# Performance work log

Hardware: AMD Instinct MI355X
Metric: run time of the kernel (lower is better)

The kernel has to match this reference:

```python
import jax, jax.numpy as jnp
import numpy as np

N = 100000   # num_nodes
E = 1600000  # num_edges
DIN = 128
H1 = 256
H2 = 128
SLOPE = 0.01  # torch leaky_relu default negative slope


def _gcn_conv(h, W, b, src, dst):
    # GCNConv: add self-loops, symmetric deg^-1/2 normalization, linear transform, scatter-add, bias
    hw = h @ W  # [N, out]
    loops = jnp.arange(N)
    s = jnp.concatenate([src, loops])
    d = jnp.concatenate([dst, loops])
    deg = jax.ops.segment_sum(jnp.ones(s.shape[0], dtype=hw.dtype), d, num_segments=N)
    dis = jnp.where(deg > 0, jax.lax.rsqrt(deg), 0.0)
    msg = hw[s] * (dis[s] * dis[d])[:, None]
    return jax.ops.segment_sum(msg, d, num_segments=N) + b


def _gru_cell(x, h, Wih, Whh, bih, bhh):
    # torch.nn.GRUCell semantics; weight layout [3H, in], gate order r, z, n
    gi = x @ Wih.T + bih
    gh = h @ Whh.T + bhh
    ir, iz, inn = jnp.split(gi, 3, axis=-1)
    hr, hz, hn = jnp.split(gh, 3, axis=-1)
    r = jax.nn.sigmoid(ir + hr)
    z = jax.nn.sigmoid(iz + hz)
    n = jnp.tanh(inn + r * hn)
    return (1.0 - z) * n + z * h


def setup_inputs() -> dict:
    key = jax.random.key(0)
    ks = jax.random.split(key, 24)
    rn = lambda k, shape, s=0.05: (jax.random.normal(k, shape) * s).astype(jnp.float32)
    return {
        "x": rn(ks[0], (N, DIN), 1.0),
        "edge_index": jax.random.randint(ks[1], (2, E), 0, N, dtype=jnp.int32),
        "prev0": rn(ks[2], (N, H1), 1.0),
        "prev1": rn(ks[3], (N, H2), 1.0),
        "Wp1": rn(ks[4], (DIN, 256)), "bp1": jnp.zeros((256,), jnp.float32),
        "Wp2": rn(ks[5], (256, 128)), "bp2": jnp.zeros((128,), jnp.float32),
        "Wc1": rn(ks[6], (128, H1)), "bc1": jnp.zeros((H1,), jnp.float32),
        "Wc2": rn(ks[7], (H1, H2)), "bc2": jnp.zeros((H2,), jnp.float32),
        "Wih1": rn(ks[8], (3 * H1, H1)), "Whh1": rn(ks[9], (3 * H1, H1)),
        "bih1": jnp.zeros((3 * H1,), jnp.float32), "bhh1": jnp.zeros((3 * H1,), jnp.float32),
        "Wih2": rn(ks[10], (3 * H2, H2)), "Whh2": rn(ks[11], (3 * H2, H2)),
        "bih2": jnp.zeros((3 * H2,), jnp.float32), "bhh2": jnp.zeros((3 * H2,), jnp.float32),
        "Wpost": rn(ks[12], (H2, 2)), "bpost": jnp.zeros((2,), jnp.float32),
    }


def reference(x, edge_index, prev0, prev1, Wp1, bp1, Wp2, bp2, Wc1, bc1, Wc2, bc2,
              Wih1, Whh1, bih1, bhh1, Wih2, Whh2, bih2, bhh2, Wpost, bpost):
    src, dst = edge_index[0], edge_index[1]
    # preprocess MLP (dropout p=0 => identity)
    h = jax.nn.leaky_relu(x @ Wp1 + bp1, SLOPE)
    h = jax.nn.leaky_relu(h @ Wp2 + bp2, SLOPE)
    # GCN layer 1 + GRU temporal update
    h = jax.nn.leaky_relu(_gcn_conv(h, Wc1, bc1, src, dst), SLOPE)
    h = _gru_cell(h, prev0, Wih1, Whh1, bih1, bhh1)
    emb0 = h
    # GCN layer 2 + GRU temporal update
    h = jax.nn.leaky_relu(_gcn_conv(h, Wc2, bc2, src, dst), SLOPE)
    h = _gru_cell(h, prev1, Wih2, Whh2, bih2, bhh2)
    emb1 = h
    # postprocess and reduce
    out = jnp.sum(h @ Wpost + bpost, axis=-1)  # [N]
    return out, emb0, emb1
```

## Files before the change

kernel.cpp:

```cpp
#include <hip/hip_runtime.h>
#include <cstdint>
#include <cstddef>

typedef __bf16 bf16x8 __attribute__((ext_vector_type(8)));
typedef float f32x4 __attribute__((ext_vector_type(4)));
typedef float f32x2 __attribute__((ext_vector_type(2)));
typedef unsigned short us16;

__device__ __forceinline__ float lrelu(float v) { return v >= 0.0f ? v : 0.01f * v; }
__device__ __forceinline__ float fsigmoid(float x) {
  x = fminf(fmaxf(x, -30.0f), 30.0f);
  return 1.0f / (1.0f + __expf(-x));
}
__device__ __forceinline__ float ftanh(float x) {
  x = fminf(fmaxf(x, -15.0f), 15.0f);
  float e = __expf(2.0f * x);
  return (e - 1.0f) / (e + 1.0f);
}
__device__ __forceinline__ us16 f2b(float f) {
  unsigned int u = __builtin_bit_cast(unsigned int, f);
  u = (u + 0x7fffu + ((u >> 16) & 1u)) >> 16;
  return (us16)u;
}
__device__ __forceinline__ float b2f(us16 h) {
  unsigned int u = ((unsigned int)h) << 16;
  return __builtin_bit_cast(float, u);
}
__device__ __forceinline__ unsigned pk2(float a, float b) {
  return (unsigned)f2b(a) | ((unsigned)f2b(b) << 16);
}
__device__ __forceinline__ unsigned char f2f8(float v) {
  return (unsigned char)(__builtin_amdgcn_cvt_pk_fp8_f32(v, v, 0, false) & 0xFF);
}
__device__ __forceinline__ void unpf8(int2 v, float* t) {
  f32x2 p0 = __builtin_amdgcn_cvt_pk_f32_fp8(v.x, false);
  f32x2 p1 = __builtin_amdgcn_cvt_pk_f32_fp8(v.x, true);
  f32x2 p2 = __builtin_amdgcn_cvt_pk_f32_fp8(v.y, false);
  f32x2 p3 = __builtin_amdgcn_cvt_pk_f32_fp8(v.y, true);
  t[0] = p0.x; t[1] = p0.y; t[2] = p1.x; t[3] = p1.y;
  t[4] = p2.x; t[5] = p2.y; t[6] = p3.x; t[7] = p3.y;
}

__device__ __forceinline__ void stage16(const us16* gsrc, us16* ldst) {
  __builtin_amdgcn_global_load_lds(
      (const __attribute__((address_space(1))) unsigned int*)(const void*)gsrc,
      (__attribute__((address_space(3))) unsigned int*)(void*)ldst, 16, 0, 0);
}
__device__ __forceinline__ bf16x8 frag_rd(const us16* base, int row, int byte_in_row) {
  int byte = row * 128 + (byte_in_row ^ ((row & 7) << 4));
  return *(const bf16x8*)((const char*)base + byte);
}
__device__ __forceinline__ bf16x8 frd32(const us16* tilebase, int row, int ck16) {
  int slot = ck16 ^ ((row >> 1) & 3);
  return *(const bf16x8*)(tilebase + row * 32 + slot * 8);
}

__global__ void k_deg(const int* __restrict__ dst, int* __restrict__ indeg, int E) {
  int e = blockIdx.x * 256 + threadIdx.x;
  if (e < E) atomicAdd(&indeg[dst[e]], 1);
}

__global__ __launch_bounds__(1024) void k_scan1(const int* __restrict__ v, int* __restrict__ rp,
                                                int* __restrict__ part, float* __restrict__ dis, int n) {
  __shared__ int wsum[16];
  int base = blockIdx.x << 10;
  int t = threadIdx.x, lane = t & 63, wv = t >> 6;
  int val = (base + t < n) ? v[base + t] : 0;
  if (base + t < n) dis[base + t] = rsqrtf((float)(val + 1));
  int s = val;
  #pragma unroll
  for (int off = 1; off < 64; off <<= 1) {
    int u = __shfl_up(s, off);
    if (lane >= off) s += u;
  }
  if (lane == 63) wsum[wv] = s;
  __syncthreads();
  int wadd = 0;
  #pragma unroll
  for (int w = 0; w < 16; ++w) wadd += (w < wv) ? wsum[w] : 0;
  if (base + t < n) rp[base + t] = wadd + s - val;
  if (t == 0) {
    int tot = 0;
    #pragma unroll
    for (int w = 0; w < 16; ++w) tot += wsum[w];
    part[blockIdx.x] = tot;
  }
}

__global__ __launch_bounds__(1024) void k_scan2(int* __restrict__ p, int nc) {
  __shared__ int wsum[16];
  int t = threadIdx.x, lane = t & 63, wv = t >> 6;
  int val = (t < nc) ? p[t] : 0;
  int s = val;
  #pragma unroll
  for (int off = 1; off < 64; off <<= 1) {
    int u = __shfl_up(s, off);
    if (lane >= off) s += u;
  }
  if (lane == 63) wsum[wv] = s;
  __syncthreads();
  int wadd = 0;
  #pragma unroll
  for (int w = 0; w < 16; ++w) wadd += (w < wv) ? wsum[w] : 0;
  if (t < nc) p[t] = wadd + s - val;
}

__global__ void k_scan3(int* __restrict__ rp, const int* __restrict__ part,
                        int* __restrict__ cursor, int n, int total) {
  int i = blockIdx.x * 256 + threadIdx.x;
  if (i < n) {
    int v = rp[i] + part[i >> 10];
    rp[i] = v;
    cursor[i] = v;
  } else if (i == n) {
    rp[n] = total;
  }
}

__global__ void k_fill(const int* __restrict__ src, const int* __restrict__ dst,
                       const float* __restrict__ dis, int* __restrict__ cursor,
                       int* __restrict__ csrc, float* __restrict__ cw, int E) {
  int e = blockIdx.x * 256 + threadIdx.x;
  if (e >= E) return;
  int s = src[e], d = dst[e];
  int pos = atomicAdd(&cursor[d], 1);
  csrc[pos] = s;
  cw[pos] = dis[s] * dis[d];
}

__global__ void k_cast(const float* __restrict__ in, us16* __restrict__ out, int n) {
  int i = (blockIdx.x * 256 + threadIdx.x) * 4;
  if (i >= n) return;
  float4 v = *(const float4*)(in + i);
  *(ushort4*)(out + i) = make_ushort4(f2b(v.x), f2b(v.y), f2b(v.z), f2b(v.w));
}

__global__ void k_prepw(const float* __restrict__ Wih1, const float* __restrict__ Whh1,
                        const float* __restrict__ Wih2, const float* __restrict__ Whh2,
                        const float* __restrict__ Wp1, const float* __restrict__ Wp2,
                        const float* __restrict__ Wc1, const float* __restrict__ Wc2,
                        us16* __restrict__ Wih1b, us16* __restrict__ Whh1b,
                        us16* __restrict__ Wih2b, us16* __restrict__ Whh2b,
                        us16* __restrict__ WtP1, us16* __restrict__ WtP2,
                        us16* __restrict__ WtC1, us16* __restrict__ WtC2) {
  int e = blockIdx.x * 256 + threadIdx.x;
  if (e < 196608) { Wih1b[e] = f2b(Wih1[e]); return; }
  e -= 196608;
  if (e < 196608) { Whh1b[e] = f2b(Whh1[e]); return; }
  e -= 196608;
  if (e < 49152) { Wih2b[e] = f2b(Wih2[e]); return; }
  e -= 49152;
  if (e < 49152) { Whh2b[e] = f2b(Whh2[e]); return; }
  e -= 49152;
  if (e < 32768) { int r = e & 127, c = e >> 7; WtP1[e] = f2b(Wp1[(size_t)r * 256 + c]); return; }
  e -= 32768;
  if (e < 32768) { int r = e & 255, c = e >> 8; WtP2[e] = f2b(Wp2[(size_t)r * 128 + c]); return; }
  e -= 32768;
  if (e < 32768) { int r = e & 127, c = e >> 7; WtC1[e] = f2b(Wc1[(size_t)r * 256 + c]); return; }
  e -= 32768;
  if (e < 32768) { int r = e & 255, c = e >> 8; WtC2[e] = f2b(Wc2[(size_t)r * 128 + c]); }
}

template<int ACT, int BIAS, int OF8>
__global__ __launch_bounds__(256) void k_mm(const us16* __restrict__ A,
                                            const us16* __restrict__ Bt,
                                            const float* __restrict__ bias,
                                            void* __restrict__ Cout,
                                            int M, int K, int Nc, int ny) {
  __shared__ __align__(16) us16 lds[2][2 * 8192];
  const int bm = (blockIdx.x / ny) * 128;
  const int bn = (blockIdx.x % ny) * 128;
  const int tid = threadIdx.x;
  const int lane = tid & 63;
  const int wave = tid >> 6;
  const int wm = (wave >> 1) * 64;
  const int wn = (wave & 1) * 64;
  const int lr = lane & 15;
  const int lk = lane >> 4;
  const int srow = lane >> 3;
  const int schk = (lane & 7) ^ srow;
  f32x4 acc[4][4] = {};

  auto stage = [&](int k0, us16* buf) {
    #pragma unroll
    for (int it = 0; it < 4; ++it) {
      int r8 = (wave * 4 + it) * 8;
      int ar = bm + r8 + srow; if (ar >= M) ar = M - 1;
      stage16(A + (size_t)ar * K + k0 + schk * 8, buf + r8 * 64);
      stage16(Bt + (size_t)(bn + r8 + srow) * K + k0 + schk * 8, buf + 8192 + r8 * 64);
    }
  };

  const int nk = K >> 6;
  stage(0, lds[0]);
  for (int t = 0; t < nk; ++t) {
    us16* cur = lds[t & 1];
    if (t + 1 < nk) {
      if (t > 0) {
        asm volatile("s_waitcnt lgkmcnt(0)" ::: "memory");
        __builtin_amdgcn_s_barrier();
      }
      stage((t + 1) << 6, lds[(t + 1) & 1]);
      asm volatile("s_waitcnt vmcnt(8)" ::: "memory");
    } else {
      asm volatile("s_waitcnt vmcnt(0)" ::: "memory");
    }
    __builtin_amdgcn_s_barrier();
    #pragma unroll
    for (int kk = 0; kk < 2; ++kk) {
      bf16x8 af[4], bq[4];
      #pragma unroll
      for (int i = 0; i < 4; ++i) af[i] = frag_rd(cur, wm + i * 16 + lr, kk * 64 + lk * 16);
      #pragma unroll
      for (int j = 0; j < 4; ++j) bq[j] = frag_rd(cur + 8192, wn + j * 16 + lr, kk * 64 + lk * 16);
      #pragma unroll
      for (int i = 0; i < 4; ++i)
        #pragma unroll
        for (int j = 0; j < 4; ++j)
          acc[i][j] = __builtin_amdgcn_mfma_f32_16x16x32_bf16(af[i], bq[j], acc[i][j], 0, 0, 0);
    }
  }
  float bb[4];
  #pragma unroll
  for (int j = 0; j < 4; ++j) bb[j] = BIAS ? bias[bn + wn + j * 16 + lr] : 0.0f;
  #pragma unroll
  for (int i = 0; i < 4; ++i) {
    #pragma unroll
    for (int q = 0; q < 4; ++q) {
      int row = bm + wm + i * 16 + lk * 4 + q;
      if (row < M) {
        #pragma unroll
        for (int j = 0; j < 4; ++j) {
          int col = bn + wn + j * 16 + lr;
          float v = acc[i][j][q] + bb[j];
          if (ACT) v = lrelu(v);
          if (OF8) ((unsigned char*)Cout)[(size_t)row * Nc + col] = f2f8(v);
          else ((us16*)Cout)[(size_t)row * Nc + col] = f2b(v);
        }
      }
    }
  }
}

template<int ACT>
__global__ __launch_bounds__(256) void k_agg128(const unsigned char* __restrict__ hw,
                                                const int* __restrict__ rp,
                                                const int* __restrict__ csrc, const float* __restrict__ cw,
                                                const float* __restrict__ dis, const float* __restrict__ bias,
                                                us16* __restrict__ outp, int M) {
  int node = blockIdx.x * 16 + (threadIdx.x >> 4);
  int l = threadIdx.x & 15;
  if (node >= M) return;
  const unsigned char* base = hw + l * 8;
  float acc[8], t0[8], t1[8], t2[8], t3[8];
  float dn = dis[node];
  float sw = dn * dn;
  {
    int2 v = *(const int2*)(base + (size_t)node * 128);
    unpf8(v, t0);
    #pragma unroll
    for (int j = 0; j < 8; ++j) acc[j] = t0[j] * sw;
  }
  int e = rp[node], e1 = rp[node + 1];
  for (; e + 4 <= e1; e += 4) {
    int s0 = csrc[e], s1 = csrc[e + 1], s2 = csrc[e + 2], s3 = csrc[e + 3];
    float w0 = cw[e], w1 = cw[e + 1], w2 = cw[e + 2], w3 = cw[e + 3];
    int2 v0 = *(const int2*)(base + (size_t)s0 * 128);
    int2 v1 = *(const int2*)(base + (size_t)s1 * 128);
    int2 v2 = *(const int2*)(base + (size_t)s2 * 128);
    int2 v3 = *(const int2*)(base + (size_t)s3 * 128);
    unpf8(v0, t0); unpf8(v1, t1); unpf8(v2, t2); unpf8(v3, t3);
    #pragma unroll
    for (int j = 0; j < 8; ++j) acc[j] = fmaf(w0, t0[j], acc[j]);
    #pragma unroll
    for (int j = 0; j < 8; ++j) acc[j] = fmaf(w1, t1[j], acc[j]);
    #pragma unroll
    for (int j = 0; j < 8; ++j) acc[j] = fmaf(w2, t2[j], acc[j]);
    #pragma unroll
    for (int j = 0; j < 8; ++j) acc[j] = fmaf(w3, t3[j], acc[j]);
  }
  for (; e < e1; ++e) {
    int s0 = csrc[e];
    float w0 = cw[e];
    int2 v0 = *(const int2*)(base + (size_t)s0 * 128);
    unpf8(v0, t0);
    #pragma unroll
    for (int j = 0; j < 8; ++j) acc[j] = fmaf(w0, t0[j], acc[j]);
  }
  if (ACT) {
    float4 b0 = *(const float4*)(bias + l * 8);
    float4 b1 = *(const float4*)(bias + l * 8 + 4);
    float bb[8] = {b0.x, b0.y, b0.z, b0.w, b1.x, b1.y, b1.z, b1.w};
    #pragma unroll
    for (int j = 0; j < 8; ++j) acc[j] = lrelu(acc[j] + bb[j]);
  }
  int4 o;
  o.x = (int)pk2(acc[0], acc[1]);
  o.y = (int)pk2(acc[2], acc[3]);
  o.z = (int)pk2(acc[4], acc[5]);
  o.w = (int)pk2(acc[6], acc[7]);
  *(int4*)(outp + (size_t)node * 128 + l * 8) = o;
}

template<int H, int WB, int PH>
__global__ __launch_bounds__(512) void k_fgru(const us16* __restrict__ xb, const us16* __restrict__ hb,
                                              const us16* __restrict__ Wih, const us16* __restrict__ Whh,
                                              const float* __restrict__ bih, const float* __restrict__ bhh,
                                              float* __restrict__ emb, us16* __restrict__ embb,
                                              const float* __restrict__ Wpost, const float* __restrict__ bpost,
                                              float* __restrict__ outv, int M, int ny) {
  __shared__ __align__(16) us16 lds[2][14336];
  const int nwg = gridDim.x;
  int bid = blockIdx.x;
  {
    int q8 = nwg >> 3, r8 = nwg & 7;
    int xc = bid & 7, ix = bid >> 3;
    bid = (xc < r8 ? xc * (q8 + 1) : r8 * (q8 + 1) + (xc - r8) * q8) + ix;
  }
  const int bn = (bid % ny) * 32;
  const int bm = (bid / ny) * 128;
  const int tid = threadIdx.x;
  const int lane = tid & 63, wave = tid >> 6;
  const int pair = wave >> 1;
  const int role = wave & 1;
  const int wm = pair * 32;
  const int lr = lane & 15, lk = lane >> 4;
  const int sl_row = lane >> 2;
  const int sl_chk = (lane & 3) ^ ((lane >> 3) & 3);

  f32x4 acc[3][2][2] = {};

  auto stage_step = [&](int k0, us16* buf) {
    #pragma unroll
    for (int it = 0; it < 4; ++it) {
      int m = wave * 4 + it;
      if (m >= 28) break;
      const us16* src;
      us16* dst;
      if (m < 16) {
        int r0 = (m & 7) * 16;
        int ar = bm + r0 + sl_row; if (ar >= M) ar = M - 1;
        src = (m < 8 ? xb : hb) + (size_t)ar * H + k0 + sl_chk * 8;
        dst = buf + (m < 8 ? 0 : 4096) + r0 * 32;
      } else {
        int wi = m - 16;
        int g6 = wi >> 1;
        int r0 = (wi & 1) * 16;
        const us16* W = (g6 < 3) ? Wih : Whh;
        int gg = (g6 < 3) ? g6 : g6 - 3;
        src = W + (size_t)(gg * H + bn + r0 + sl_row) * H + k0 + sl_chk * 8;
        dst = buf + 8192 + g6 * 1024 + r0 * 32;
      }
      stage16(src, dst);
    }
  };

  const int nk = H >> 5;
  stage_step(0, lds[0]);
  for (int t = 0; t < nk; ++t) {
    us16* cur = lds[t & 1];
    if (t + 1 < nk) {
      if (t > 0) {
        asm volatile("s_waitcnt lgkmcnt(0)" ::: "memory");
        __builtin_amdgcn_s_barrier();
      }
      stage_step((t + 1) << 5, lds[(t + 1) & 1]);
      asm volatile("s_waitcnt vmcnt(4)" ::: "memory");
    } else {
      asm volatile("s_waitcnt vmcnt(0)" ::: "memory");
    }
    __builtin_amdgcn_s_barrier();
    const us16* at = cur + (role ? 4096 : 0);
    bf16x8 a0 = frd32(at, wm + lr, lk);
    bf16x8 a1 = frd32(at, wm + 16 + lr, lk);
    #pragma unroll
    for (int g = 0; g < 3; ++g) {
      const us16* wt = cur + 8192 + (role * 3 + g) * 1024;
      bf16x8 b0 = frd32(wt, lr, lk);
      bf16x8 b1 = frd32(wt, 16 + lr, lk);
      acc[g][0][0] = __builtin_amdgcn_mfma_f32_16x16x32_bf16(a0, b0, acc[g][0][0], 0, 0, 0);
      acc[g][0][1] = __builtin_amdgcn_mfma_f32_16x16x32_bf16(a0, b1, acc[g][0][1], 0, 0, 0);
      acc[g][1][0] = __builtin_amdgcn_mfma_f32_16x16x32_bf16(a1, b0, acc[g][1][0], 0, 0, 0);
      acc[g][1][1] = __builtin_amdgcn_mfma_f32_16x16x32_bf16(a1, b1, acc[g][1][1], 0, 0, 0);
    }
  }
  __syncthreads();
  float* xch = (float*)&lds[0][0];
  if (role) {
    #pragma unroll
    for (int g = 0; g < 3; ++g)
      #pragma unroll
      for (int i = 0; i < 2; ++i)
        #pragma unroll
        for (int j = 0; j < 2; ++j)
          *(f32x4*)&xch[((((pair * 3 + g) * 2 + i) * 2 + j) * 64 + lane) * 4] = acc[g][i][j];
  }
  __syncthreads();
  if (!role) {
    float part[2][4] = {};
    #pragma unroll
    for (int j = 0; j < 2; ++j) {
      int col = bn + j * 16 + lr;
      float bir = bih[col], biz = bih[H + col], bin = bih[2 * H + col];
      float bhr = bhh[col], bhz = bhh[H + col], bhn = bhh[2 * H + col];
      float wps = 0.0f;
      if (PH) wps = Wpost[2 * col] + Wpost[2 * col + 1];
      #pragma unroll
      for (int i = 0; i < 2; ++i) {
        f32x4 gr_ = *(const f32x4*)&xch[((((pair * 3 + 0) * 2 + i) * 2 + j) * 64 + lane) * 4];
        f32x4 gz_ = *(const f32x4*)&xch[((((pair * 3 + 1) * 2 + i) * 2 + j) * 64 + lane) * 4];
        f32x4 gn_ = *(const f32x4*)&xch[((((pair * 3 + 2) * 2 + i) * 2 + j) * 64 + lane) * 4];
        #pragma unroll
        for (int q = 0; q < 4; ++q) {
          int row = bm + wm + i * 16 + lk * 4 + q;
          if (row < M) {
            float r = fsigmoid(acc[0][i][j][q] + bir + gr_[q] + bhr);
            float z = fsigmoid(acc[1][i][j][q] + biz + gz_[q] + bhz);
            float n = ftanh(acc[2][i][j][q] + bin + r * (gn_[q] + bhn));
            float hv = b2f(hb[(size_t)row * H + col]);
            float o = (1.0f - z) * n + z * hv;
            emb[(size_t)row * H + col] = o;
            if (WB) embb[(size_t)row * H + col] = f2b(o);
            if (PH) part[i][q] += o * wps;
          }
        }
      }
    }
    if (PH) {
      float bsum = bpost[0] + bpost[1];
      #pragma unroll
      for (int i = 0; i < 2; ++i)
        #pragma unroll
        for (int q = 0; q < 4; ++q) {
          float v = part[i][q];
          v += __shfl_xor(v, 1); v += __shfl_xor(v, 2);
          v += __shfl_xor(v, 4); v += __shfl_xor(v, 8);
          int row = bm + wm + i * 16 + lk * 4 + q;
          if (lr == 0 && row < M)
            atomicAdd(&outv[row], v + (bn == 0 ? bsum : 0.0f));
        }
    }
  }
}

extern "C" void kernel_launch(void* const* d_in, const int* in_sizes, int n_in,
                              void* d_out, int out_size, void* d_ws, size_t ws_size,
                              hipStream_t stream) {
  const float* x     = (const float*)d_in[0];
  const int*   ei    = (const int*)d_in[1];
  const float* prev0 = (const float*)d_in[2];
  const float* prev1 = (const float*)d_in[3];
  const float* Wp1   = (const float*)d_in[4];
  const float* bp1   = (const float*)d_in[5];
  const float* Wp2   = (const float*)d_in[6];
  const float* bp2   = (const float*)d_in[7];
  const float* Wc1   = (const float*)d_in[8];
  const float* bc1   = (const float*)d_in[9];
  const float* Wc2   = (const float*)d_in[10];
  const float* bc2   = (const float*)d_in[11];
  const float* Wih1  = (const float*)d_in[12];
  const float* Whh1  = (const float*)d_in[13];
  const float* bih1  = (const float*)d_in[14];
  const float* bhh1  = (const float*)d_in[15];
  const float* Wih2  = (const float*)d_in[16];
  const float* Whh2  = (const float*)d_in[17];
  const float* bih2  = (const float*)d_in[18];
  const float* bhh2  = (const float*)d_in[19];
  const float* Wpost = (const float*)d_in[20];
  const float* bpost = (const float*)d_in[21];

  const int N = in_sizes[0] / 128;
  const int E = in_sizes[1] / 2;
  const int* srcp = ei;
  const int* dstp = ei + E;

  char* wsb = (char*)d_ws;
  size_t off = 0;
  auto alloc = [&](size_t bytes) -> void* {
    void* p = wsb + off;
    off = (off + bytes + 255) & ~(size_t)255;
    return p;
  };
  float* dis    = (float*)alloc((size_t)N * 4);
  int*   indeg  = (int*)alloc((size_t)N * 4);
  int*   rp     = (int*)alloc((size_t)(N + 1) * 4);
  int*   part   = (int*)alloc((size_t)1024 * 4);
  int*   cursor = (int*)alloc((size_t)N * 4);
  int*   csrc   = (int*)alloc((size_t)E * 4);
  float* cw     = (float*)alloc((size_t)E * 4);
  us16* xb    = (us16*)alloc((size_t)N * 128 * 2);
  us16* p0b   = (us16*)alloc((size_t)N * 256 * 2);
  us16* p1b   = (us16*)alloc((size_t)N * 128 * 2);
  us16* WtP1  = (us16*)alloc((size_t)256 * 128 * 2);
  us16* WtP2  = (us16*)alloc((size_t)128 * 256 * 2);
  us16* WtC1  = (us16*)alloc((size_t)256 * 128 * 2);
  us16* WtC2  = (us16*)alloc((size_t)128 * 256 * 2);
  us16* Wih1b = (us16*)alloc((size_t)768 * 256 * 2);
  us16* Whh1b = (us16*)alloc((size_t)768 * 256 * 2);
  us16* Wih2b = (us16*)alloc((size_t)384 * 128 * 2);
  us16* Whh2b = (us16*)alloc((size_t)384 * 128 * 2);
  us16* bufA  = (us16*)alloc((size_t)N * 256 * 2);
  unsigned char* buf8 = (unsigned char*)alloc((size_t)N * 128);
  us16* bufD  = (us16*)alloc((size_t)N * 128 * 2);
  us16* emb0b = (us16*)alloc((size_t)N * 256 * 2);
  (void)ws_size; (void)n_in; (void)out_size;

  float* outv = (float*)d_out;
  float* emb0 = outv + N;
  float* emb1 = emb0 + (size_t)N * 256;

  auto cg = [](long n) { return (unsigned)((n / 4 + 255) / 256); };

  hipMemsetAsync(outv, 0, (size_t)N * 4, stream);

  k_cast<<<cg((long)N * 128), 256, 0, stream>>>(x, xb, N * 128);
  k_cast<<<cg((long)N * 256), 256, 0, stream>>>(prev0, p0b, N * 256);
  k_cast<<<cg((long)N * 128), 256, 0, stream>>>(prev1, p1b, N * 128);
  k_prepw<<<2432, 256, 0, stream>>>(Wih1, Whh1, Wih2, Whh2, Wp1, Wp2, Wc1, Wc2,
                                    Wih1b, Whh1b, Wih2b, Whh2b, WtP1, WtP2, WtC1, WtC2);

  hipMemsetAsync(indeg, 0, (size_t)N * 4, stream);
  k_deg<<<(E + 255) / 256, 256, 0, stream>>>(dstp, indeg, E);
  const int NC = (N + 1023) / 1024;
  k_scan1<<<NC, 1024, 0, stream>>>(indeg, rp, part, dis, N);
  k_scan2<<<1, 1024, 0, stream>>>(part, NC);
  k_scan3<<<(N + 256) / 256, 256, 0, stream>>>(rp, part, cursor, N, E);
  k_fill<<<(E + 255) / 256, 256, 0, stream>>>(srcp, dstp, dis, cursor, csrc, cw, E);

  const int MB = (N + 127) / 128;
  const int AB = (N + 15) / 16;

  k_mm<1, 1, 0><<<MB * 2, 256, 0, stream>>>(xb, WtP1, bp1, bufA, N, 128, 256, 2);
  k_mm<1, 1, 1><<<MB, 256, 0, stream>>>(bufA, WtP2, bp2, buf8, N, 256, 128, 1);
  k_agg128<0><<<AB, 256, 0, stream>>>(buf8, rp, csrc, cw, dis, nullptr, bufD, N);
  k_mm<1, 1, 0><<<MB * 2, 256, 0, stream>>>(bufD, WtC1, bc1, bufA, N, 128, 256, 2);
  k_fgru<256, 1, 0><<<MB * 8, 512, 0, stream>>>(bufA, p0b, Wih1b, Whh1b, bih1, bhh1,
                                                emb0, emb0b, nullptr, nullptr, nullptr, N, 8);
  k_mm<0, 0, 1><<<MB, 256, 0, stream>>>(emb0b, WtC2, nullptr, buf8, N, 256, 128, 1);
  k_agg128<1><<<AB, 256, 0, stream>>>(buf8, rp, csrc, cw, dis, bc2, bufD, N);
  k_fgru<128, 0, 1><<<MB * 4, 512, 0, stream>>>(bufD, p1b, Wih2b, Whh2b, bih2, bhh2,
                                                emb1, nullptr, Wpost, bpost, outv, N, 4);
}
```

Baseline: 749.6 us.

## Widen fused GRU tile to 64 columns and merge input cast kernels

The fused GRU kernel now computes 64 output columns per workgroup instead of 32. Each wave holds a 64x32 accumulator tile, so the staged x/h row tiles are reused across twice as many columns and the grid shrinks by half. The epilogue exchange runs in two phases because of the larger accumulator set. The three activation cast kernels are merged into one launch. The cost is larger LDS use (about 80KB), more accumulator registers per wave, and fewer workgroups, all of which may lower occupancy.

```diff
diff --git a/kernel.cpp b/kernel.cpp
--- a/kernel.cpp
+++ b/kernel.cpp
@@ -128,11 +128,21 @@
   cw[pos] = dis[s] * dis[d];
 }
 
-__global__ void k_cast(const float* __restrict__ in, us16* __restrict__ out, int n) {
+__global__ void k_castall(const float* __restrict__ x, const float* __restrict__ p0,
+                          const float* __restrict__ p1,
+                          us16* __restrict__ xb, us16* __restrict__ p0b,
+                          us16* __restrict__ p1b, int N) {
   int i = (blockIdx.x * 256 + threadIdx.x) * 4;
-  if (i >= n) return;
-  float4 v = *(const float4*)(in + i);
-  *(ushort4*)(out + i) = make_ushort4(f2b(v.x), f2b(v.y), f2b(v.z), f2b(v.w));
+  const int nx = N * 128, n0 = N * 256;
+  const float* src;
+  us16* dst;
+  int off;
+  if (i < nx) { src = x; dst = xb; off = i; }
+  else if (i < nx + n0) { src = p0; dst = p0b; off = i - nx; }
+  else if (i < nx + n0 + nx) { src = p1; dst = p1b; off = i - nx - n0; }
+  else return;
+  float4 v = *(const float4*)(src + off);
+  *(ushort4*)(dst + off) = make_ushort4(f2b(v.x), f2b(v.y), f2b(v.z), f2b(v.w));
 }
 
 __global__ void k_prepw(const float* __restrict__ Wih1, const float* __restrict__ Whh1,
@@ -309,7 +319,7 @@
                                               float* __restrict__ emb, us16* __restrict__ embb,
                                               const float* __restrict__ Wpost, const float* __restrict__ bpost,
                                               float* __restrict__ outv, int M, int ny) {
-  __shared__ __align__(16) us16 lds[2][14336];
+  __shared__ __align__(16) us16 lds[2][20480];
   const int nwg = gridDim.x;
   int bid = blockIdx.x;
   {
@@ -317,24 +327,23 @@
     int xc = bid & 7, ix = bid >> 3;
     bid = (xc < r8 ? xc * (q8 + 1) : r8 * (q8 + 1) + (xc - r8) * q8) + ix;
   }
-  const int bn = (bid % ny) * 32;
+  const int bn = (bid % ny) * 64;
   const int bm = (bid / ny) * 128;
   const int tid = threadIdx.x;
   const int lane = tid & 63, wave = tid >> 6;
-  const int pair = wave >> 1;
-  const int role = wave & 1;
-  const int wm = pair * 32;
+  const int pair = wave >> 2;
+  const int role = (wave >> 1) & 1;
+  const int ch = wave & 1;
   const int lr = lane & 15, lk = lane >> 4;
   const int sl_row = lane >> 2;
   const int sl_chk = (lane & 3) ^ ((lane >> 3) & 3);
 
-  f32x4 acc[3][2][2] = {};
+  f32x4 acc[3][4][2] = {};
 
   auto stage_step = [&](int k0, us16* buf) {
     #pragma unroll
-    for (int it = 0; it < 4; ++it) {
-      int m = wave * 4 + it;
-      if (m >= 28) break;
+    for (int it = 0; it < 5; ++it) {
+      int m = wave * 5 + it;
       const us16* src;
       us16* dst;
       if (m < 16) {
@@ -344,12 +353,12 @@
         dst = buf + (m < 8 ? 0 : 4096) + r0 * 32;
       } else {
         int wi = m - 16;
-        int g6 = wi >> 1;
-        int r0 = (wi & 1) * 16;
+        int g6 = wi >> 2;
+        int r0 = (wi & 3) * 16;
         const us16* W = (g6 < 3) ? Wih : Whh;
         int gg = (g6 < 3) ? g6 : g6 - 3;
         src = W + (size_t)(gg * H + bn + r0 + sl_row) * H + k0 + sl_chk * 8;
-        dst = buf + 8192 + g6 * 1024 + r0 * 32;
+        dst = buf + 8192 + g6 * 2048 + r0 * 32;
       }
       stage16(src, dst);
     }
@@ -365,80 +374,85 @@
         __builtin_amdgcn_s_barrier();
       }
       stage_step((t + 1) << 5, lds[(t + 1) & 1]);
-      asm volatile("s_waitcnt vmcnt(4)" ::: "memory");
+      asm volatile("s_waitcnt vmcnt(5)" ::: "memory");
     } else {
       asm volatile("s_waitcnt vmcnt(0)" ::: "memory");
     }
     __builtin_amdgcn_s_barrier();
     const us16* at = cur + (role ? 4096 : 0);
-    bf16x8 a0 = frd32(at, wm + lr, lk);
-    bf16x8 a1 = frd32(at, wm + 16 + lr, lk);
+    bf16x8 a[4];
+    #pragma unroll
+    for (int i = 0; i < 4; ++i) a[i] = frd32(at, pair * 64 + i * 16 + lr, lk);
     #pragma unroll
     for (int g = 0; g < 3; ++g) {
-      const us16* wt = cur + 8192 + (role * 3 + g) * 1024;
-      bf16x8 b0 = frd32(wt, lr, lk);
-      bf16x8 b1 = frd32(wt, 16 + lr, lk);
-      acc[g][0][0] = __builtin_amdgcn_mfma_f32_16x16x32_bf16(a0, b0, acc[g][0][0], 0, 0, 0);
-      acc[g][0][1] = __builtin_amdgcn_mfma_f32_16x16x32_bf16(a0, b1, acc[g][0][1], 0, 0, 0);
-      acc[g][1][0] = __builtin_amdgcn_mfma_f32_16x16x32_bf16(a1, b0, acc[g][1][0], 0, 0, 0);
-      acc[g][1][1] = __builtin_amdgcn_mfma_f32_16x16x32_bf16(a1, b1, acc[g][1][1], 0, 0, 0);
-    }
-  }
-  __syncthreads();
+      const us16* wt = cur + 8192 + (role * 3 + g) * 2048;
+      bf16x8 b0 = frd32(wt, ch * 32 + lr, lk);
+      bf16x8 b1 = frd32(wt, ch * 32 + 16 + lr, lk);
+      #pragma unroll
+      for (int i = 0; i < 4; ++i) {
+        acc[g][i][0] = __builtin_amdgcn_mfma_f32_16x16x32_bf16(a[i], b0, acc[g][i][0], 0, 0, 0);
+        acc[g][i][1] = __builtin_amdgcn_mfma_f32_16x16x32_bf16(a[i], b1, acc[g][i][1], 0, 0, 0);
+      }
+    }
+  }
   float* xch = (float*)&lds[0][0];
-  if (role) {
-    #pragma unroll
-    for (int g = 0; g < 3; ++g)
+  #pragma unroll
+  for (int ph = 0; ph < 2; ++ph) {
+    __syncthreads();
+    if (role == 1 && ch == ph) {
       #pragma unroll
-      for (int i = 0; i < 2; ++i)
+      for (int g = 0; g < 3; ++g)
         #pragma unroll
-        for (int j = 0; j < 2; ++j)
-          *(f32x4*)&xch[((((pair * 3 + g) * 2 + i) * 2 + j) * 64 + lane) * 4] = acc[g][i][j];
-  }
-  __syncthreads();
-  if (!role) {
-    float part[2][4] = {};
-    #pragma unroll
-    for (int j = 0; j < 2; ++j) {
-      int col = bn + j * 16 + lr;
-      float bir = bih[col], biz = bih[H + col], bin = bih[2 * H + col];
-      float bhr = bhh[col], bhz = bhh[H + col], bhn = bhh[2 * H + col];
-      float wps = 0.0f;
-      if (PH) wps = Wpost[2 * col] + Wpost[2 * col + 1];
+        for (int i = 0; i < 4; ++i)
+          #pragma unroll
+          for (int j = 0; j < 2; ++j)
+            *(f32x4*)&xch[((((pair * 3 + g) * 4 + i) * 2 + j) * 64 + lane) * 4] = acc[g][i][j];
+    }
+    __syncthreads();
+    if (role == 0 && ch == ph) {
+      float part[4][4] = {};
       #pragma unroll
-      for (int i = 0; i < 2; ++i) {
-        f32x4 gr_ = *(const f32x4*)&xch[((((pair * 3 + 0) * 2 + i) * 2 + j) * 64 + lane) * 4];
-        f32x4 gz_ = *(const f32x4*)&xch[((((pair * 3 + 1) * 2 + i) * 2 + j) * 64 + lane) * 4];
-        f32x4 gn_ = *(const f32x4*)&xch[((((pair * 3 + 2) * 2 + i) * 2 + j) * 64 + lane) * 4];
+      for (int j = 0; j < 2; ++j) {
+        int col = bn + ch * 32 + j * 16 + lr;
+        float bir = bih[col], biz = bih[H + col], bin = bih[2 * H + col];
+        float bhr = bhh[col], bhz = bhh[H + col], bhn = bhh[2 * H + col];
+        float wps = 0.0f;
+        if (PH) wps = Wpost[2 * col] + Wpost[2 * col + 1];
         #pragma unroll
-        for (int q = 0; q < 4; ++q) {
-          int row = bm + wm + i * 16 + lk * 4 + q;
-          if (row < M) {
-            float r = fsigmoid(acc[0][i][j][q] + bir + gr_[q] + bhr);
-            float z = fsigmoid(acc[1][i][j][q] + biz + gz_[q] + bhz);
-            float n = ftanh(acc[2][i][j][q] + bin + r * (gn_[q] + bhn));
-            float hv = b2f(hb[(size_t)row * H + col]);
-            float o = (1.0f - z) * n + z * hv;
-            emb[(size_t)row * H + col] = o;
-            if (WB) embb[(size_t)row * H + col] = f2b(o);
-            if (PH) part[i][q] += o * wps;
+        for (int i = 0; i < 4; ++i) {
+          f32x4 gr_ = *(const f32x4*)&xch[((((pair * 3 + 0) * 4 + i) * 2 + j) * 64 + lane) * 4];
+          f32x4 gz_ = *(const f32x4*)&xch[((((pair * 3 + 1) * 4 + i) * 2 + j) * 64 + lane) * 4];
+          f32x4 gn_ = *(const f32x4*)&xch[((((pair * 3 + 2) * 4 + i) * 2 + j) * 64 + lane) * 4];
+          #pragma unroll
+          for (int q = 0; q < 4; ++q) {
+            int row = bm + pair * 64 + i * 16 + lk * 4 + q;
+            if (row < M) {
+              float r = fsigmoid(acc[0][i][j][q] + bir + gr_[q] + bhr);
+              float z = fsigmoid(acc[1][i][j][q] + biz + gz_[q] + bhz);
+              float n = ftanh(acc[2][i][j][q] + bin + r * (gn_[q] + bhn));
+              float hv = b2f(hb[(size_t)row * H + col]);
+              float o = (1.0f - z) * n + z * hv;
+              emb[(size_t)row * H + col] = o;
+              if (WB) embb[(size_t)row * H + col] = f2b(o);
+              if (PH) part[i][q] += o * wps;
+            }
           }
         }
       }
-    }
-    if (PH) {
-      float bsum = bpost[0] + bpost[1];
-      #pragma unroll
-      for (int i = 0; i < 2; ++i)
+      if (PH) {
+        float bsum = bpost[0] + bpost[1];
         #pragma unroll
-        for (int q = 0; q < 4; ++q) {
-          float v = part[i][q];
-          v += __shfl_xor(v, 1); v += __shfl_xor(v, 2);
-          v += __shfl_xor(v, 4); v += __shfl_xor(v, 8);
-          int row = bm + wm + i * 16 + lk * 4 + q;
-          if (lr == 0 && row < M)
-            atomicAdd(&outv[row], v + (bn == 0 ? bsum : 0.0f));
-        }
+        for (int i = 0; i < 4; ++i)
+          #pragma unroll
+          for (int q = 0; q < 4; ++q) {
+            float v = part[i][q];
+            v += __shfl_xor(v, 1); v += __shfl_xor(v, 2);
+            v += __shfl_xor(v, 4); v += __shfl_xor(v, 8);
+            int row = bm + pair * 64 + i * 16 + lk * 4 + q;
+            if (lr == 0 && row < M)
+              atomicAdd(&outv[row], v + ((bn == 0 && ch == 0) ? bsum : 0.0f));
+          }
+      }
     }
   }
 }
@@ -509,13 +523,9 @@
   float* emb0 = outv + N;
   float* emb1 = emb0 + (size_t)N * 256;
 
-  auto cg = [](long n) { return (unsigned)((n / 4 + 255) / 256); };
-
   hipMemsetAsync(outv, 0, (size_t)N * 4, stream);
 
-  k_cast<<<cg((long)N * 128), 256, 0, stream>>>(x, xb, N * 128);
-  k_cast<<<cg((long)N * 256), 256, 0, stream>>>(prev0, p0b, N * 256);
-  k_cast<<<cg((long)N * 128), 256, 0, stream>>>(prev1, p1b, N * 128);
+  k_castall<<<((size_t)N * 512 / 4 + 255) / 256, 256, 0, stream>>>(x, prev0, prev1, xb, p0b, p1b, N);
   k_prepw<<<2432, 256, 0, stream>>>(Wih1, Whh1, Wih2, Whh2, Wp1, Wp2, Wc1, Wc2,
                                     Wih1b, Whh1b, Wih2b, Whh2b, WtP1, WtP2, WtC1, WtC2);
 
@@ -534,10 +544,10 @@
   k_mm<1, 1, 1><<<MB, 256, 0, stream>>>(bufA, WtP2, bp2, buf8, N, 256, 128, 1);
   k_agg128<0><<<AB, 256, 0, stream>>>(buf8, rp, csrc, cw, dis, nullptr, bufD, N);
   k_mm<1, 1, 0><<<MB * 2, 256, 0, stream>>>(bufD, WtC1, bc1, bufA, N, 128, 256, 2);
-  k_fgru<256, 1, 0><<<MB * 8, 512, 0, stream>>>(bufA, p0b, Wih1b, Whh1b, bih1, bhh1,
-                                                emb0, emb0b, nullptr, nullptr, nullptr, N, 8);
+  k_fgru<256, 1, 0><<<MB * 4, 512, 0, stream>>>(bufA, p0b, Wih1b, Whh1b, bih1, bhh1,
+                                                emb0, emb0b, nullptr, nullptr, nullptr, N, 4);
   k_mm<0, 0, 1><<<MB, 256, 0, stream>>>(emb0b, WtC2, nullptr, buf8, N, 256, 128, 1);
   k_agg128<1><<<AB, 256, 0, stream>>>(buf8, rp, csrc, cw, dis, bc2, bufD, N);
-  k_fgru<128, 0, 1><<<MB * 4, 512, 0, stream>>>(bufD, p1b, Wih2b, Whh2b, bih2, bhh2,
-                                                emb1, nullptr, Wpost, bpost, outv, N, 4);
-}
+  k_fgru<128, 0, 1><<<MB * 2, 512, 0, stream>>>(bufD, p1b, Wih2b, Whh2b, bih2, bhh2,
+                                                emb1, nullptr, Wpost, bpost, outv, N, 2);
+}
```

Result: slower. 1.160 ms (+54.7%).
